# Optimization experiments

Measured on AMD Instinct MI355X. Metric: run time of the kernel, lower is better.

## Reference

```python
import jax, jax.numpy as jnp
import numpy as np
import math

B, C, H, WIN = 8, 96, 224, 7
D_STATE, DT_RANK = 16, 6
PERK = C // 4
K_RATIO = 0.25


def nearest_perfect_square(val):
    if val <= 0:
        return 0
    s = math.sqrt(val)
    lo = math.floor(s) ** 2
    hi = math.ceil(s) ** 2
    return lo if abs(lo - val) <= abs(hi - val) else hi


def setup_inputs() -> dict:
    key = jax.random.key(0)
    ks = jax.random.split(key, 8)
    x = jax.random.normal(ks[0], (B, C, H, H), dtype=jnp.float32)
    router_w1 = jax.random.normal(ks[1], (C // 4, C), jnp.float32) * (1.0 / math.sqrt(C))
    router_b1 = jnp.zeros((C // 4,), jnp.float32)
    router_w2 = jax.random.normal(ks[2], (1, C // 4), jnp.float32) * (1.0 / math.sqrt(C // 4))
    router_b2 = jnp.zeros((1,), jnp.float32)
    x_proj_weight = jax.random.normal(ks[3], (4, DT_RANK + 2 * D_STATE, PERK), jnp.float32) * (1.0 / math.sqrt(PERK))
    std = DT_RANK ** -0.5
    dt_projs_weight = jax.random.uniform(ks[4], (4, PERK, DT_RANK), jnp.float32, -std, std)
    dt = jnp.exp(jax.random.uniform(ks[5], (4, PERK), jnp.float32) * (math.log(0.1) - math.log(0.001)) + math.log(0.001))
    dt = jnp.clip(dt, 1e-4)
    dt_projs_bias = dt + jnp.log(-jnp.expm1(-dt))  # inv-softplus init as in dt_init_fn
    A_logs = jnp.log(jnp.tile(jnp.arange(1, D_STATE + 1, dtype=jnp.float32)[None, :], (4 * PERK, 1)))
    Ds = jnp.ones((4 * PERK,), jnp.float32)
    return {"x": x, "router_w1": router_w1, "router_b1": router_b1, "router_w2": router_w2,
            "router_b2": router_b2, "x_proj_weight": x_proj_weight, "dt_projs_weight": dt_projs_weight,
            "dt_projs_bias": dt_projs_bias, "A_logs": A_logs, "Ds": Ds}


def reference(x, router_w1, router_b1, router_w2, router_b2, x_proj_weight,
              dt_projs_weight, dt_projs_bias, A_logs, Ds):
    Bb, Cc, Hh, Ww = x.shape
    nH = Hh // WIN
    N = nH * nH
    # window partition: b c (nh p1) (nw p2) -> b (nh nw) c p1 p2
    windows = x.reshape(Bb, Cc, nH, WIN, nH, WIN).transpose(0, 2, 4, 1, 3, 5).reshape(Bb, N, Cc, WIN, WIN)
    # router scores
    pooled = windows.mean(axis=(-2, -1))  # [B,N,C]
    hid = jax.nn.gelu(pooled @ router_w1.T + router_b1, approximate=False)
    logits = (hid @ router_w2.T + router_b2)[..., 0]  # [B,N]
    probs = jax.nn.softmax(logits, axis=1)
    top_k = min(max(nearest_perfect_square(N * K_RATIO), 1), N)
    n = int(math.isqrt(top_k))
    rw, sel = jax.lax.top_k(probs, top_k)  # sorted descending, like torch.topk
    windows_flat = windows.reshape(Bb, N, -1)
    cur = jnp.take_along_axis(windows_flat, sel[:, :, None], axis=1)  # [B,topk,C*w*w]
    cur = cur.reshape(Bb, n, n, Cc, WIN, WIN)
    L = n * n * WIN * WIN
    # channel interleave (p k) -> (k p), k=4
    x_int = cur.reshape(Bb, n, n, Cc // 4, 4, WIN, WIN).transpose(0, 1, 2, 4, 3, 5, 6)  # [B,n,n,4,perK,w,w]

    def local_scan(w, column_first, flip):
        # w: [B,n,n,D,wh,ww] -> [B,D,L]
        if column_first:
            w = w.transpose(0, 3, 2, 1, 5, 4)
        else:
            w = w.transpose(0, 3, 1, 2, 4, 5)
        w = w.reshape(Bb, -1, L)
        if flip:
            w = w[..., ::-1]
        return w

    xs = jnp.stack([
        local_scan(x_int[:, :, :, 0], False, False),
        local_scan(x_int[:, :, :, 1], True, False),
        local_scan(x_int[:, :, :, 2], False, True),
        local_scan(x_int[:, :, :, 3], True, True),
    ], axis=1)  # [B,4,perK,L]

    x_dbl = jnp.einsum('bkdl,kcd->bkcl', xs, x_proj_weight)
    dts = x_dbl[:, :, :DT_RANK]
    Bmat = x_dbl[:, :, DT_RANK:DT_RANK + D_STATE]  # [B,4,Nst,L]
    Cmat = x_dbl[:, :, DT_RANK + D_STATE:]
    dts = jnp.einsum('bkrl,kdr->bkdl', dts, dt_projs_weight)  # [B,4,perK,L]
    A_g = -jnp.exp(A_logs).reshape(4, PERK, D_STATE)
    delta = jax.nn.softplus(dts + dt_projs_bias.reshape(4, PERK)[None, :, :, None])

    # selective scan (grouped): h_{l} = exp(delta*A)*h_{l-1} + delta*u*B_l ; y_l = <h_l, C_l>
    dl = jnp.moveaxis(delta, -1, 0)  # [L,B,4,perK]
    ul = jnp.moveaxis(xs, -1, 0)
    Bl = jnp.moveaxis(Bmat, -1, 0)   # [L,B,4,Nst]
    Cl = jnp.moveaxis(Cmat, -1, 0)
    h0 = jnp.zeros((Bb, 4, PERK, D_STATE), jnp.float32)

    def step(h, inp):
        d, u, Bt, Ct = inp
        h = jnp.exp(d[..., None] * A_g) * h + (d * u)[..., None] * Bt[:, :, None, :]
        return h, jnp.einsum('bkdn,bkn->bkd', h, Ct)

    _, ys = jax.lax.scan(step, h0, (dl, ul, Bl, Cl))
    y = jnp.moveaxis(ys, 0, -1) + xs * Ds.reshape(4, PERK)[None, :, :, None]  # [B,4,perK,L]

    def local_reverse(yk, column_first, flip):
        if flip:
            yk = yk[..., ::-1]
        if column_first:
            yk = yk.reshape(Bb, -1, n, n, WIN, WIN).transpose(0, 1, 3, 5, 2, 4).reshape(Bb, -1, L)
        else:
            yk = yk.reshape(Bb, -1, n, n, WIN, WIN).transpose(0, 1, 2, 4, 3, 5).reshape(Bb, -1, L)
        return yk

    yout = jnp.concatenate([
        local_reverse(y[:, 0], False, False),
        local_reverse(y[:, 1], True, False),
        local_reverse(y[:, 2], False, True),
        local_reverse(y[:, 3], True, True),
    ], axis=1)  # [B,C,L]
    yout = yout.reshape(Bb, Cc, n * n, WIN * WIN).transpose(0, 2, 1, 3).reshape(Bb, top_k, -1)
    cur_out = yout * rw[:, :, None]
    residual = windows_flat * probs[:, :, None]
    residual = residual.at[jnp.arange(Bb)[:, None], sel].set(cur_out)
    new = windows_flat + residual
    return new.reshape(Bb, Cc, -1)
```

## Files before the change

### kernel.cpp

```cpp
#include <hip/hip_runtime.h>
#include <math.h>

#define BBATCH 8
#define CC 96
#define HH 224
#define NHW 32
#define NWIN 1024
#define TOPK 256
#define PERK 24
#define DST 16
#define DTR 6
#define LL 12544
#define LCP 52
#define NG 13
#define TCH 256
#define NBK 32
#define XROW 1248
#define WST2 2912

#define OFF_POOL 0
#define OFF_PROB 794624
#define OFF_RW   802816
#define OFF_RANK 804864
#define OFF_SEL  813056
#define OFF_WEFF 815104
#define OFF_CP   820480
#define OFF_CS   3966208
#define OFF_XSD  7111936
#define OFF_STG  17335552

#define ROR_ADD(v, CTRL) \
    v += __int_as_float(__builtin_amdgcn_update_dpp(0, __float_as_int(v), CTRL, 0xf, 0xf, true))

__global__ void k_pool(const float* __restrict__ x, float* __restrict__ pooled) {
    int bc = blockIdx.x;
    const float* xp = x + (size_t)bc * HH * HH;
    float* pp = pooled + (size_t)bc * NWIN;
    for (int w = threadIdx.x; w < NWIN; w += blockDim.x) {
        int wr = w >> 5, wc = w & 31;
        const float* base = xp + (wr * 7) * HH + wc * 7;
        float s = 0.f;
        #pragma unroll
        for (int i = 0; i < 7; ++i) {
            #pragma unroll
            for (int j = 0; j < 7; ++j) s += base[i * HH + j];
        }
        pp[w] = s * (1.0f / 49.0f);
    }
}

__global__ __launch_bounds__(1024) void k_route(
        const float* __restrict__ pooled,
        const float* __restrict__ w1, const float* __restrict__ b1,
        const float* __restrict__ w2, const float* __restrict__ b2,
        const float* __restrict__ xpw, const float* __restrict__ dtw,
        float* __restrict__ wcomb, float* __restrict__ probs) {
    __shared__ float sw1[PERK * CC];
    __shared__ float sb1[PERK];
    __shared__ float sw2[PERK];
    __shared__ float red[NWIN];
    int b = blockIdx.x, t = threadIdx.x;
    for (int i = b * 1024 + t; i < 4 * 56 * PERK; i += 8 * 1024) {
        int k = i / (56 * PERK), rem = i - k * (56 * PERK);
        int row = rem / PERK, c = rem - row * PERK;
        float v;
        if (row < PERK) {
            v = 0.f;
            #pragma unroll
            for (int r = 0; r < DTR; ++r)
                v += dtw[(k * PERK + row) * DTR + r] * xpw[(k * 38 + r) * PERK + c];
        } else {
            v = xpw[(k * 38 + (row - PERK + DTR)) * PERK + c];
        }
        wcomb[i] = v;
    }
    for (int i = t; i < PERK * CC; i += 1024) sw1[i] = w1[i];
    if (t < PERK) { sb1[t] = b1[t]; sw2[t] = w2[t]; }
    __syncthreads();
    float hid[PERK];
    #pragma unroll
    for (int j = 0; j < PERK; ++j) hid[j] = sb1[j];
    const float* pp = pooled + (size_t)b * CC * NWIN + t;
    for (int c = 0; c < CC; ++c) {
        float pv = pp[(size_t)c * NWIN];
        #pragma unroll
        for (int j = 0; j < PERK; ++j) hid[j] += pv * sw1[j * CC + c];
    }
    float lg = b2[0];
    #pragma unroll
    for (int j = 0; j < PERK; ++j) {
        float hv = hid[j];
        float g = 0.5f * hv * (1.0f + erff(hv * 0.7071067811865476f));
        lg += g * sw2[j];
    }
    red[t] = lg; __syncthreads();
    for (int o = 512; o > 0; o >>= 1) { if (t < o) red[t] = fmaxf(red[t], red[t + o]); __syncthreads(); }
    float mx = red[0]; __syncthreads();
    float e = expf(lg - mx);
    red[t] = e; __syncthreads();
    for (int o = 512; o > 0; o >>= 1) { if (t < o) red[t] += red[t + o]; __syncthreads(); }
    probs[b * NWIN + t] = e / red[0];
}

__global__ __launch_bounds__(64) void k_rank2(const float* __restrict__ probs,
        float* __restrict__ rw, int* __restrict__ rank, int* __restrict__ sel) {
    __shared__ __attribute__((aligned(16))) float sp[NWIN];
    int b = blockIdx.x >> 4, slice = blockIdx.x & 15;
    int tid = threadIdx.x;
    for (int i = tid; i < NWIN / 4; i += 64)
        ((float4*)sp)[i] = ((const float4*)(probs + (size_t)b * NWIN))[i];
    __syncthreads();
    int w = slice * 64 + tid;
    float p = sp[w];
    int r = 0;
    for (int j = 0; j < NWIN; j += 4) {
        float4 pj = *(const float4*)&sp[j];
        r += (int)((pj.x > p) || (pj.x == p && (j + 0) < w));
        r += (int)((pj.y > p) || (pj.y == p && (j + 1) < w));
        r += (int)((pj.z > p) || (pj.z == p && (j + 2) < w));
        r += (int)((pj.w > p) || (pj.w == p && (j + 3) < w));
    }
    rank[b * NWIN + w] = r;
    if (r < TOPK) { sel[b * TOPK + r] = w; rw[b * TOPK + r] = p; }
}

__device__ __forceinline__ float softplus_f(float v) {
    return fmaxf(v, 0.f) + __logf(1.0f + __expf(-fabsf(v)));
}

__device__ __forceinline__ int window_wsel(const int* sel, int b, int k, int t) {
    int qscan = (k >= 2) ? (255 - t) : t;
    int selidx = (k & 1) ? (((qscan & 15) << 4) | (qscan >> 4)) : qscan;
    return sel[b * TOPK + selidx];
}

__global__ __launch_bounds__(256) void k_gather(const float* __restrict__ x,
        const int* __restrict__ sel, float* __restrict__ xsd) {
    const int total = NBK * TCH * XROW;
    for (int e = blockIdx.x * 256 + threadIdx.x; e < total; e += gridDim.x * 256) {
        int blk = e / XROW;
        int rem = e - blk * XROW;
        int d2 = rem / LCP, j = rem - d2 * LCP;
        float v = 0.f;
        if (j < 49) {
            int t = blk & 255, bk = blk >> 8, k = bk & 3, b = bk >> 2;
            int wsel = window_wsel(sel, b, k, t);
            int pix = (k >= 2) ? 48 - j : j;
            int q7 = pix / 7, r7 = pix - q7 * 7;
            int wi = (k & 1) ? r7 : q7;
            int wj = (k & 1) ? q7 : r7;
            v = x[(((size_t)b * CC + 4 * d2 + k) * HH + (wsel >> 5) * 7 + wi) * HH
                  + (wsel & 31) * 7 + wj];
        }
        xsd[e] = v;
    }
}

__global__ __launch_bounds__(384, 4) void k_prodD(
        const float* __restrict__ xsd, const float* __restrict__ wcomb,
        const float* __restrict__ dtb, const float* __restrict__ alogs,
        float* __restrict__ stage, float* __restrict__ carrP, float* __restrict__ carrS) {
    __shared__ __attribute__((aligned(16))) float sxs[PERK][LCP];
    __shared__ __attribute__((aligned(16))) float sprj[56][LCP];
    __shared__ float swt[56 * PERK];
    __shared__ float sbias[PERK];
    int blk = blockIdx.x;
    int bk = blk >> 8; int k = bk & 3;
    int tid = threadIdx.x;
    const float4* xin = (const float4*)(xsd + (size_t)blk * XROW);
    for (int i = tid; i < XROW / 4; i += 384) ((float4*)sxs)[i] = xin[i];
    for (int i = tid; i < 56 * PERK; i += 384) swt[i] = wcomb[k * (56 * PERK) + i];
    if (tid < PERK) sbias[tid] = dtb[k * PERK + tid];
    if (tid < 168) {
        int r = tid / 3, j = 49 + tid % 3;
        sprj[r][j] = 0.f;
    }
    int d = tid >> 4, s = tid & 15;
    float A = -__expf(alogs[(k * PERK + d) * DST + s]);
    __syncthreads();
    for (int idx = tid; idx < 56 * NG; idx += 384) {
        int row = idx / NG, g = idx - row * NG; int j = g * 4;
        float bs = (row < PERK) ? sbias[row] : 0.f;
        float ax = bs, ay = bs, az = bs, aw = bs;
        #pragma unroll
        for (int d2 = 0; d2 < PERK; ++d2) {
            float w = swt[row * PERK + d2];
            float4 v = *(const float4*)&sxs[d2][j];
            ax += w * v.x; ay += w * v.y; az += w * v.z; aw += w * v.w;
        }
        if (row < PERK) {
            ax = softplus_f(ax); ay = softplus_f(ay); az = softplus_f(az); aw = softplus_f(aw);
        }
        float* dst = &sprj[row][j];
        if (g < 12) { float4 o = {ax, ay, az, aw}; *(float4*)dst = o; }
        else dst[0] = ax;
    }
    __syncthreads();
    float4* sg = (float4*)(stage + (size_t)blk * WST2);
    const float4* sp4 = (const float4*)&sprj[0][0];
    for (int i = tid; i < WST2 / 4; i += 384) sg[i] = sp4[i];
    float P = 1.f, S = 0.f;
    for (int g = 0; g < NG; ++g) {
        int j = g * 4;
        float4 dl4 = *(const float4*)&sprj[d][j];
        float4 xs4 = *(const float4*)&sxs[d][j];
        float4 B4  = *(const float4*)&sprj[24 + s][j];
        float aa;
        aa = __expf(dl4.x * A); S = aa * S + (dl4.x * xs4.x) * B4.x; P *= aa;
        aa = __expf(dl4.y * A); S = aa * S + (dl4.y * xs4.y) * B4.y; P *= aa;
        aa = __expf(dl4.z * A); S = aa * S + (dl4.z * xs4.z) * B4.z; P *= aa;
        aa = __expf(dl4.w * A); S = aa * S + (dl4.w * xs4.w) * B4.w; P *= aa;
    }
    size_t cidx = (size_t)blk * 384 + tid;
    carrP[cidx] = P; carrS[cidx] = S;
}

__global__ void k_carry(const float* carrP, const float* carrS, float* hin) {
    int gid = blockIdx.x * blockDim.x + threadIdx.x;
    int bk = gid / 384, ds = gid - bk * 384;
    float Hv = 0.f;
    for (int t = 0; t < TCH; ++t) {
        size_t idx = ((size_t)bk * TCH + t) * 384 + ds;
        float pv = carrP[idx], sv = carrS[idx];
        hin[idx] = Hv;
        Hv = pv * Hv + sv;
    }
}

__global__ __launch_bounds__(64) void k_base(const float* __restrict__ x,
        const float* __restrict__ probs, const int* __restrict__ rank,
        float* __restrict__ out) {
    int wr = blockIdx.x % NHW; int bc = blockIdx.x / NHW;
    int b = bc / CC;
    __shared__ float buf[7 * HH];
    __shared__ float fmul[NHW];
    __shared__ int   fsel[NHW];
    int tid = threadIdx.x;
    const float* xp = x + ((size_t)bc * HH + wr * 7) * HH;
    for (int i = tid; i < 7 * HH; i += 64) buf[i] = xp[i];
    if (tid < NHW) {
        int w = wr * NHW + tid;
        fsel[tid] = (rank[b * NWIN + w] < TOPK);
        fmul[tid] = 1.0f + probs[b * NWIN + w];
    }
    __syncthreads();
    int c = bc - b * CC;
    for (int idx = tid; idx < NHW * 49; idx += 64) {
        int wc = idx / 49, r = idx - wc * 49;
        if (fsel[wc]) continue;
        int ri = r / 7, rj = r - ri * 7;
        float v = buf[ri * HH + wc * 7 + rj];
        int w = wr * NHW + wc;
        out[(((size_t)b * NWIN + w) * CC + c) * 49 + r] = v * fmul[wc];
    }
}

__global__ __launch_bounds__(384, 4) void k_scan2(
        const float* __restrict__ alogs, const float* __restrict__ dsv,
        const float* __restrict__ hin, const float* __restrict__ xsd,
        float* __restrict__ stage) {
    __shared__ __attribute__((aligned(16))) float sy[PERK][LCP];
    int blk = blockIdx.x;
    int bk = blk >> 8; int k = bk & 3;
    int tid = threadIdx.x;
    int d = tid >> 4, s = tid & 15;
    float A = -__expf(alogs[(k * PERK + d) * DST + s]);
    float Dsr = dsv[k * PERK + d];
    size_t cidx = (size_t)blk * 384 + tid;
    float h = hin[cidx];
    const float* sg = stage + (size_t)blk * WST2;
    const float* pdl = sg + d * LCP;
    const float* pB  = sg + (24 + s) * LCP;
    const float* pC  = sg + (40 + s) * LCP;
    const float* pxs = xsd + (size_t)blk * XROW + d * LCP;
    float4 dlC = *(const float4*)(pdl);     float4 xsC = *(const float4*)(pxs);
    float4 BC_ = *(const float4*)(pB);      float4 CC_ = *(const float4*)(pC);
    float4 dlN = *(const float4*)(pdl + 4); float4 xsN = *(const float4*)(pxs + 4);
    float4 BN_ = *(const float4*)(pB + 4);  float4 CN_ = *(const float4*)(pC + 4);
    for (int g = 0; g < NG; ++g) {
        float4 dl4 = dlC, xs4 = xsC, B4 = BC_, C4 = CC_;
        dlC = dlN; xsC = xsN; BC_ = BN_; CC_ = CN_;
        if (g + 2 < NG) {
            int jn = (g + 2) * 4;
            dlN = *(const float4*)(pdl + jn); xsN = *(const float4*)(pxs + jn);
            BN_ = *(const float4*)(pB + jn);  CN_ = *(const float4*)(pC + jn);
        }
        int j = g * 4;
        float aa, part;
        aa = __expf(dl4.x * A); h = aa * h + (dl4.x * xs4.x) * B4.x;
        part = h * C4.x;
        ROR_ADD(part, 0x121); ROR_ADD(part, 0x122); ROR_ADD(part, 0x124); ROR_ADD(part, 0x128);
        if (s == 0) sy[d][j] = part + xs4.x * Dsr;
        aa = __expf(dl4.y * A); h = aa * h + (dl4.y * xs4.y) * B4.y;
        part = h * C4.y;
        ROR_ADD(part, 0x121); ROR_ADD(part, 0x122); ROR_ADD(part, 0x124); ROR_ADD(part, 0x128);
        if (s == 0 && j + 1 < 49) sy[d][j + 1] = part + xs4.y * Dsr;
        aa = __expf(dl4.z * A); h = aa * h + (dl4.z * xs4.z) * B4.z;
        part = h * C4.z;
        ROR_ADD(part, 0x121); ROR_ADD(part, 0x122); ROR_ADD(part, 0x124); ROR_ADD(part, 0x128);
        if (s == 0 && j + 2 < 49) sy[d][j + 2] = part + xs4.z * Dsr;
        aa = __expf(dl4.w * A); h = aa * h + (dl4.w * xs4.w) * B4.w;
        part = h * C4.w;
        ROR_ADD(part, 0x121); ROR_ADD(part, 0x122); ROR_ADD(part, 0x124); ROR_ADD(part, 0x128);
        if (s == 0 && j + 3 < 49) sy[d][j + 3] = part + xs4.w * Dsr;
    }
    __syncthreads();
    float* yout = stage + (size_t)blk * WST2;
    for (int idx = tid; idx < PERK * 49; idx += 384) {
        int j = idx / PERK, d2 = idx - j * PERK;
        yout[idx] = sy[d2][j];
    }
}

__global__ __launch_bounds__(256) void k_yadd(const float* __restrict__ stage,
        const float* __restrict__ x, const int* __restrict__ sel,
        const float* __restrict__ rw, float* __restrict__ out) {
    __shared__ float ytile[CC * 49];
    int qo = blockIdx.x & 255; int b = blockIdx.x >> 8;
    int wsel = sel[b * TOPK + qo];
    float p = rw[b * TOPK + qo];
    for (int idx = threadIdx.x; idx < CC * 49; idx += 256) {
        int k = idx / 1176; int r1 = idx - k * 1176;
        int u = r1 / 168;   int r2 = r1 - u * 168;
        int wj = r2 / 24;   int d = r2 - wj * 24;
        int rest = qo * 7 + u;
        int b2 = rest & 15; int aw = rest >> 4;
        int wi = aw % 7;    int a = aw / 7;
        int q   = (k & 1) ? (b2 * 16 + a) : (a * 16 + b2);
        int pix = (k & 1) ? (wj * 7 + wi) : (wi * 7 + wj);
        int uu = q * 49 + pix;
        int l = (k >= 2) ? (LL - 1 - uu) : uu;
        int bk = b * 4 + k;
        int t2 = l / 49, jj = l - t2 * 49;
        ytile[(k * PERK + d) * 49 + u * 7 + wj] =
            p * stage[((size_t)(bk * 256 + t2)) * WST2 + jj * PERK + d];
    }
    __syncthreads();
    float* ob = out + ((size_t)(b * NWIN + wsel) * CC) * 49;
    int gi0 = (wsel >> 5) * 7, gj0 = (wsel & 31) * 7;
    for (int e = threadIdx.x; e < CC * 49; e += 256) {
        int C = e / 49, cell = e - C * 49;
        int u = cell / 7, wj = cell - u * 7;
        float xv = x[(((size_t)b * CC + C) * HH + gi0 + u) * HH + gj0 + wj];
        ob[e] = xv + ytile[e];
    }
}

extern "C" void kernel_launch(void* const* d_in, const int* in_sizes, int n_in,
                              void* d_out, int out_size, void* d_ws, size_t ws_size,
                              hipStream_t stream) {
    const float* x   = (const float*)d_in[0];
    const float* w1  = (const float*)d_in[1];
    const float* b1  = (const float*)d_in[2];
    const float* w2  = (const float*)d_in[3];
    const float* b2  = (const float*)d_in[4];
    const float* xpw = (const float*)d_in[5];
    const float* dtw = (const float*)d_in[6];
    const float* dtb = (const float*)d_in[7];
    const float* alg = (const float*)d_in[8];
    const float* dsv = (const float*)d_in[9];
    float* out = (float*)d_out;
    float* ws  = (float*)d_ws;

    float* pooled = ws + OFF_POOL;
    float* probs  = ws + OFF_PROB;
    float* rwv    = ws + OFF_RW;
    int*   rank   = (int*)(ws + OFF_RANK);
    int*   sel    = (int*)(ws + OFF_SEL);
    float* wcomb  = ws + OFF_WEFF;
    float* cP  = ws + OFF_CP;
    float* cS  = ws + OFF_CS;
    float* xsd = ws + OFF_XSD;
    float* stage = ws + OFF_STG;

    k_pool  <<<BBATCH * CC, 256, 0, stream>>>(x, pooled);
    k_route <<<BBATCH, 1024, 0, stream>>>(pooled, w1, b1, w2, b2, xpw, dtw, wcomb, probs);
    k_rank2 <<<BBATCH * 16, 64, 0, stream>>>(probs, rwv, rank, sel);
    k_gather<<<2048, 256, 0, stream>>>(x, sel, xsd);
    k_prodD <<<NBK * TCH, 384, 0, stream>>>(xsd, wcomb, dtb, alg, stage, cP, cS);
    k_carry <<<48, 256, 0, stream>>>(cP, cS, cP);
    k_base  <<<BBATCH * CC * NHW, 64, 0, stream>>>(x, probs, rank, out);
    k_scan2 <<<NBK * TCH, 384, 0, stream>>>(alg, dsv, cP, xsd, stage);
    k_yadd  <<<BBATCH * TOPK, 256, 0, stream>>>(stage, x, sel, rwv, out);
}
```

Baseline: 505.0 us.

## Split router into wide logits kernel and move softmax into rank kernel

The single 8-block, 1024-thread router kernel is split up. A 128-block, 64-thread kernel now computes the logits. The rank kernel computes the softmax redundantly in each block, then ranks as before. The weight-combination precompute moves to its own small kernel. The goal is to spread the serial router work over more compute units, at the cost of one extra launch and repeated softmax reductions in every rank block.

```diff
diff --git a/kernel.cpp b/kernel.cpp
--- a/kernel.cpp
+++ b/kernel.cpp
@@ -19,6 +19,7 @@
 #define WST2 2912
 
 #define OFF_POOL 0
+#define OFF_LOG  786432
 #define OFF_PROB 794624
 #define OFF_RW   802816
 #define OFF_RANK 804864
@@ -31,6 +32,24 @@
 
 #define ROR_ADD(v, CTRL) \
     v += __int_as_float(__builtin_amdgcn_update_dpp(0, __float_as_int(v), CTRL, 0xf, 0xf, true))
+
+__global__ void k_weff(const float* __restrict__ xpw, const float* __restrict__ dtw,
+                       float* __restrict__ wcomb) {
+    int i = blockIdx.x * blockDim.x + threadIdx.x;
+    if (i >= 4 * 56 * PERK) return;
+    int k = i / (56 * PERK), rem = i - k * (56 * PERK);
+    int row = rem / PERK, c = rem - row * PERK;
+    float v;
+    if (row < PERK) {
+        v = 0.f;
+        #pragma unroll
+        for (int r = 0; r < DTR; ++r)
+            v += dtw[(k * PERK + row) * DTR + r] * xpw[(k * 38 + r) * PERK + c];
+    } else {
+        v = xpw[(k * 38 + (row - PERK + DTR)) * PERK + c];
+    }
+    wcomb[i] = v;
+}
 
 __global__ void k_pool(const float* __restrict__ x, float* __restrict__ pooled) {
     int bc = blockIdx.x;
@@ -49,38 +68,24 @@
     }
 }
 
-__global__ __launch_bounds__(1024) void k_route(
+__global__ __launch_bounds__(64) void k_router(
         const float* __restrict__ pooled,
         const float* __restrict__ w1, const float* __restrict__ b1,
         const float* __restrict__ w2, const float* __restrict__ b2,
-        const float* __restrict__ xpw, const float* __restrict__ dtw,
-        float* __restrict__ wcomb, float* __restrict__ probs) {
+        float* __restrict__ logits) {
     __shared__ float sw1[PERK * CC];
     __shared__ float sb1[PERK];
     __shared__ float sw2[PERK];
-    __shared__ float red[NWIN];
-    int b = blockIdx.x, t = threadIdx.x;
-    for (int i = b * 1024 + t; i < 4 * 56 * PERK; i += 8 * 1024) {
-        int k = i / (56 * PERK), rem = i - k * (56 * PERK);
-        int row = rem / PERK, c = rem - row * PERK;
-        float v;
-        if (row < PERK) {
-            v = 0.f;
-            #pragma unroll
-            for (int r = 0; r < DTR; ++r)
-                v += dtw[(k * PERK + row) * DTR + r] * xpw[(k * 38 + r) * PERK + c];
-        } else {
-            v = xpw[(k * 38 + (row - PERK + DTR)) * PERK + c];
-        }
-        wcomb[i] = v;
-    }
-    for (int i = t; i < PERK * CC; i += 1024) sw1[i] = w1[i];
-    if (t < PERK) { sb1[t] = b1[t]; sw2[t] = w2[t]; }
-    __syncthreads();
+    int b = blockIdx.x >> 4, slice = blockIdx.x & 15;
+    int tid = threadIdx.x;
+    for (int i = tid; i < PERK * CC; i += 64) sw1[i] = w1[i];
+    if (tid < PERK) { sb1[tid] = b1[tid]; sw2[tid] = w2[tid]; }
+    __syncthreads();
+    int w = slice * 64 + tid;
     float hid[PERK];
     #pragma unroll
     for (int j = 0; j < PERK; ++j) hid[j] = sb1[j];
-    const float* pp = pooled + (size_t)b * CC * NWIN + t;
+    const float* pp = pooled + (size_t)b * CC * NWIN + w;
     for (int c = 0; c < CC; ++c) {
         float pv = pp[(size_t)c * NWIN];
         #pragma unroll
@@ -93,25 +98,36 @@
         float g = 0.5f * hv * (1.0f + erff(hv * 0.7071067811865476f));
         lg += g * sw2[j];
     }
-    red[t] = lg; __syncthreads();
-    for (int o = 512; o > 0; o >>= 1) { if (t < o) red[t] = fmaxf(red[t], red[t + o]); __syncthreads(); }
-    float mx = red[0]; __syncthreads();
-    float e = expf(lg - mx);
-    red[t] = e; __syncthreads();
-    for (int o = 512; o > 0; o >>= 1) { if (t < o) red[t] += red[t + o]; __syncthreads(); }
-    probs[b * NWIN + t] = e / red[0];
-}
-
-__global__ __launch_bounds__(64) void k_rank2(const float* __restrict__ probs,
-        float* __restrict__ rw, int* __restrict__ rank, int* __restrict__ sel) {
+    logits[b * NWIN + w] = lg;
+}
+
+__global__ __launch_bounds__(64) void k_rankF(const float* __restrict__ logits,
+        float* __restrict__ probs, float* __restrict__ rw,
+        int* __restrict__ rank, int* __restrict__ sel) {
     __shared__ __attribute__((aligned(16))) float sp[NWIN];
+    __shared__ float red[64];
     int b = blockIdx.x >> 4, slice = blockIdx.x & 15;
     int tid = threadIdx.x;
     for (int i = tid; i < NWIN / 4; i += 64)
-        ((float4*)sp)[i] = ((const float4*)(probs + (size_t)b * NWIN))[i];
+        ((float4*)sp)[i] = ((const float4*)(logits + (size_t)b * NWIN))[i];
+    __syncthreads();
+    float m = -1e30f;
+    for (int i = tid; i < NWIN; i += 64) m = fmaxf(m, sp[i]);
+    red[tid] = m; __syncthreads();
+    for (int o = 32; o > 0; o >>= 1) { if (tid < o) red[tid] = fmaxf(red[tid], red[tid + o]); __syncthreads(); }
+    float mx = red[0]; __syncthreads();
+    for (int i = tid; i < NWIN; i += 64) sp[i] = expf(sp[i] - mx);
+    __syncthreads();
+    float s = 0.f;
+    for (int i = tid; i < NWIN; i += 64) s += sp[i];
+    red[tid] = s; __syncthreads();
+    for (int o = 32; o > 0; o >>= 1) { if (tid < o) red[tid] += red[tid + o]; __syncthreads(); }
+    float sum = red[0]; __syncthreads();
+    for (int i = tid; i < NWIN; i += 64) sp[i] = sp[i] / sum;
     __syncthreads();
     int w = slice * 64 + tid;
     float p = sp[w];
+    probs[b * NWIN + w] = p;
     int r = 0;
     for (int j = 0; j < NWIN; j += 4) {
         float4 pj = *(const float4*)&sp[j];
@@ -363,6 +379,7 @@
     float* ws  = (float*)d_ws;
 
     float* pooled = ws + OFF_POOL;
+    float* logits = ws + OFF_LOG;
     float* probs  = ws + OFF_PROB;
     float* rwv    = ws + OFF_RW;
     int*   rank   = (int*)(ws + OFF_RANK);
@@ -374,8 +391,9 @@
     float* stage = ws + OFF_STG;
 
     k_pool  <<<BBATCH * CC, 256, 0, stream>>>(x, pooled);
-    k_route <<<BBATCH, 1024, 0, stream>>>(pooled, w1, b1, w2, b2, xpw, dtw, wcomb, probs);
-    k_rank2 <<<BBATCH * 16, 64, 0, stream>>>(probs, rwv, rank, sel);
+    k_router<<<BBATCH * 16, 64, 0, stream>>>(pooled, w1, b1, w2, b2, logits);
+    k_rankF <<<BBATCH * 16, 64, 0, stream>>>(logits, probs, rwv, rank, sel);
+    k_weff  <<<(4 * 56 * PERK + 255) / 256, 256, 0, stream>>>(xpw, dtw, wcomb);
     k_gather<<<2048, 256, 0, stream>>>(x, sel, xsd);
     k_prodD <<<NBK * TCH, 384, 0, stream>>>(xsd, wcomb, dtb, alg, stage, cP, cS);
     k_carry <<<48, 256, 0, stream>>>(cP, cS, cP);
```

Result: faster. 487.8 us (-3.4%).
